# Kernel tuning notes

Measured on AMD Instinct MI355X. Metric: run time of the kernel, lower is better.

The kernel has to match this reference:

```python
import jax, jax.numpy as jnp
import numpy as np

LAMBDA_M = 1.0
NUM_GRU_LAYERS = 3

B, S, H, G = 64, 512, 768, 768


def setup_inputs() -> dict:
    key = jax.random.key(0)
    ks = jax.random.split(key, 12)
    std = 0.02
    # variable-length attention mask (all rows non-empty)
    lengths = jax.random.randint(ks[0], (B,), S // 4, S + 1)
    attention_mask = (jnp.arange(S)[None, :] < lengths[:, None]).astype(jnp.float32)
    return {
        "sentence_representation": jax.random.normal(ks[1], (B, H), jnp.float32),
        "attention_mask": attention_mask,
        "aspect_embedding": jax.random.normal(ks[2], (B, H), jnp.float32),
        "sentence_embeddings": jax.random.normal(ks[3], (B, S, H), jnp.float32),
        "ws": std * jax.random.normal(ks[4], (H, H), jnp.float32),
        "wa": std * jax.random.normal(ks[5], (H, H), jnp.float32),
        "w": std * jax.random.normal(ks[6], (H,), jnp.float32),
        "whs": std * jax.random.normal(ks[7], (H, G), jnp.float32),
        "wd1": std * jax.random.normal(ks[8], (H, H), jnp.float32),
        "wd": std * jax.random.normal(ks[9], (G, H), jnp.float32),
        "w_ih": std * jax.random.normal(ks[10], (3 * G, H), jnp.float32),  # GRU input weights (r,z,n)
        "w_hh": std * jax.random.normal(ks[11], (3 * G, G), jnp.float32),  # GRU hidden weights (r,z,n)
    }


def _gru_cell(x, h, w_ih, w_hh):
    # standard GRU cell, bias=False (torch gate order: r, z, n)
    gi = x @ w_ih.T  # (B, 3G)
    gh = h @ w_hh.T  # (B, 3G)
    i_r, i_z, i_n = jnp.split(gi, 3, axis=-1)
    h_r, h_z, h_n = jnp.split(gh, 3, axis=-1)
    r = jax.nn.sigmoid(i_r + h_r)
    z = jax.nn.sigmoid(i_z + h_z)
    n = jnp.tanh(i_n + r * h_n)
    return (1.0 - z) * n + z * h


def reference(sentence_representation, attention_mask, aspect_embedding,
              sentence_embeddings, ws, wa, w, whs, wd1, wd, w_ih, w_hh):
    # Hoist loop-invariant projections (same math as recomputing per layer)
    Se = jnp.einsum('bsh,hk->bsk', sentence_embeddings, ws)  # (B,S,H)
    A = aspect_embedding @ wa                                 # (B,H)
    mask = attention_mask                                     # (B,S)
    denom = mask.sum(-1, keepdims=True)                       # (B,1)
    h = sentence_representation
    for t in range(NUM_GRU_LAYERS):
        Wd = wd1 if t == 0 else wd
        M = Se + (h @ Wd)[:, None, :] + A[:, None, :]         # (B,S,H)
        scores = jnp.tanh(M) @ w                              # (B,S)
        m = jax.nn.softmax(LAMBDA_M * scores, axis=-1)        # (B,S)
        # reweighted masked-mean pooling
        at = jnp.einsum('bs,bsh->bh', m * mask, sentence_embeddings) / denom
        if t == 0:
            h = h @ whs                                       # project to GRU hidden dim
        h = _gru_cell(at, h, w_ih, w_hh)
    return h
```

## Files before the change

### kernel.cpp

```cpp
#include <hip/hip_runtime.h>
#include <hip/hip_bf16.h>
#include <stdint.h>

#define Bdim 64
#define Sdim 512
#define Hdim 768
#define G3   2304

typedef float f32x4 __attribute__((ext_vector_type(4)));
typedef short s16x8 __attribute__((ext_vector_type(8)));
typedef short s16x4 __attribute__((ext_vector_type(4)));

__device__ __forceinline__ float bf2f(unsigned short u){
  union { unsigned int i; float f; } c; c.i = ((unsigned int)u) << 16; return c.f;
}
__device__ __forceinline__ float bflo(unsigned int x){
  union { unsigned int i; float f; } c; c.i = x << 16; return c.f;
}
__device__ __forceinline__ float bfhi(unsigned int x){
  union { unsigned int i; float f; } c; c.i = x & 0xffff0000u; return c.f;
}
__device__ __forceinline__ unsigned short f2bf(float f){
  union { float f; unsigned int i; } c; c.f = f;
  unsigned int x = c.i;
  return (unsigned short)((x + 0x7fffu + ((x >> 16) & 1u)) >> 16);
}
__device__ __forceinline__ float fast_tanh(float x){
  float e = __expf(2.f * x);
  return 1.f - 2.f / (e + 1.f);
}
__device__ __forceinline__ float fast_sigmoid(float x){
  return 1.f / (1.f + __expf(-x));
}
__device__ __forceinline__ void gload16(const void* g, void* l){
  __builtin_amdgcn_global_load_lds((const __attribute__((address_space(1))) void*)g,
                                   (__attribute__((address_space(3))) void*)l, 16, 0, 0);
}

__global__ __launch_bounds__(256) void k_prep(const float* __restrict__ SE, unsigned short* __restrict__ SEb,
                                              const float* __restrict__ ws_, unsigned short* __restrict__ wsbT,
                                              const float* __restrict__ wd1, unsigned short* __restrict__ wd1T,
                                              const float* __restrict__ wd,  unsigned short* __restrict__ wdT,
                                              const float* __restrict__ wa,  unsigned short* __restrict__ waT,
                                              const float* __restrict__ whs, unsigned short* __restrict__ whsT,
                                              const float* __restrict__ w_ih, unsigned short* __restrict__ w_ihb,
                                              const float* __restrict__ w_hh, unsigned short* __restrict__ w_hhb,
                                              const float* __restrict__ sr,  unsigned short* __restrict__ srb,
                                              const float* __restrict__ asp, unsigned short* __restrict__ aspb){
  __shared__ float tile[64][65];
  int bid = blockIdx.x;
  if (bid < 720) {
    int which = bid / 144, r = bid % 144;
    const float* src; unsigned short* dst;
    switch (which) {
      case 0: src = ws_; dst = wsbT; break;
      case 1: src = wd1; dst = wd1T; break;
      case 2: src = wd;  dst = wdT;  break;
      case 3: src = wa;  dst = waT;  break;
      default: src = whs; dst = whsT; break;
    }
    int bx = (r % 12) * 64, by = (r / 12) * 64;
    int tx = threadIdx.x % 64, ty = threadIdx.x / 64;
    #pragma unroll
    for (int j = ty; j < 64; j += 4) tile[j][tx] = src[(size_t)(by + j) * Hdim + bx + tx];
    __syncthreads();
    #pragma unroll
    for (int j = ty; j < 64; j += 4) dst[(size_t)(bx + j) * Hdim + by + tx] = f2bf(tile[tx][j]);
    return;
  }
  bid -= 720;
  const float* s; unsigned short* d; int j;
  if      (bid < 12288) { s = SE;   d = SEb;   j = bid * 256 + threadIdx.x; }
  else if (bid < 13152) { s = w_ih; d = w_ihb; j = (bid - 12288) * 256 + threadIdx.x; }
  else if (bid < 14016) { s = w_hh; d = w_hhb; j = (bid - 13152) * 256 + threadIdx.x; }
  else if (bid < 14040) { s = sr;   d = srb;   j = (bid - 14016) * 256 + threadIdx.x; }
  else                  { s = asp;  d = aspb;  j = (bid - 14040) * 256 + threadIdx.x; }
  const float4* sp = (const float4*)s;
  float4 a = sp[2*j], b = sp[2*j+1];
  uint4 o;
  o.x = (unsigned)f2bf(a.x) | ((unsigned)f2bf(a.y) << 16);
  o.y = (unsigned)f2bf(a.z) | ((unsigned)f2bf(a.w) << 16);
  o.z = (unsigned)f2bf(b.x) | ((unsigned)f2bf(b.y) << 16);
  o.w = (unsigned)f2bf(b.z) | ((unsigned)f2bf(b.w) << 16);
  ((uint4*)d)[j] = o;
}

__global__ __launch_bounds__(256) void k_conv_bf16(const float* __restrict__ src,
                                                   unsigned short* __restrict__ dst, int n8){
  int i = blockIdx.x * 256 + threadIdx.x;
  if (i >= n8) return;
  const float4* s = (const float4*)src;
  float4 a = s[2*i], b = s[2*i+1];
  uint4 o;
  o.x = (unsigned)f2bf(a.x) | ((unsigned)f2bf(a.y) << 16);
  o.y = (unsigned)f2bf(a.z) | ((unsigned)f2bf(a.w) << 16);
  o.z = (unsigned)f2bf(b.x) | ((unsigned)f2bf(b.y) << 16);
  o.w = (unsigned)f2bf(b.z) | ((unsigned)f2bf(b.w) << 16);
  ((uint4*)dst)[i] = o;
}

__global__ __launch_bounds__(256) void k_conv4(const float* __restrict__ s0, unsigned short* __restrict__ d0, int c0,
                                               const float* __restrict__ s1, unsigned short* __restrict__ d1, int c1,
                                               const float* __restrict__ s2, unsigned short* __restrict__ d2, int c2,
                                               const float* __restrict__ s3, unsigned short* __restrict__ d3, int c3){
  int i = blockIdx.x * 256 + threadIdx.x;
  const float* s; unsigned short* d; int j;
  if (i < c0) { s = s0; d = d0; j = i; }
  else if (i < c0 + c1) { s = s1; d = d1; j = i - c0; }
  else if (i < c0 + c1 + c2) { s = s2; d = d2; j = i - c0 - c1; }
  else if (i < c0 + c1 + c2 + c3) { s = s3; d = d3; j = i - c0 - c1 - c2; }
  else return;
  const float4* sp = (const float4*)s;
  float4 a = sp[2*j], b = sp[2*j+1];
  uint4 o;
  o.x = (unsigned)f2bf(a.x) | ((unsigned)f2bf(a.y) << 16);
  o.y = (unsigned)f2bf(a.z) | ((unsigned)f2bf(a.w) << 16);
  o.z = (unsigned)f2bf(b.x) | ((unsigned)f2bf(b.y) << 16);
  o.w = (unsigned)f2bf(b.z) | ((unsigned)f2bf(b.w) << 16);
  ((uint4*)d)[j] = o;
}

__global__ __launch_bounds__(256) void k_transpose_ws(const float* __restrict__ src,
                                                      unsigned short* __restrict__ dst){
  __shared__ float tile[32][33];
  int bx = blockIdx.x * 32, by = blockIdx.y * 32;
  int tx = threadIdx.x % 32, ty = threadIdx.x / 32;
  for (int j = ty; j < 32; j += 8) tile[j][tx] = src[(size_t)(by + j) * Hdim + bx + tx];
  __syncthreads();
  for (int j = ty; j < 32; j += 8) dst[(size_t)(bx + j) * Hdim + by + tx] = f2bf(tile[tx][j]);
}

__global__ __launch_bounds__(256) void k_transpose4(const float* __restrict__ s0, unsigned short* __restrict__ d0,
                                                    const float* __restrict__ s1, unsigned short* __restrict__ d1,
                                                    const float* __restrict__ s2, unsigned short* __restrict__ d2,
                                                    const float* __restrict__ s3, unsigned short* __restrict__ d3){
  const float* src; unsigned short* dst;
  switch (blockIdx.z) {
    case 0: src = s0; dst = d0; break;
    case 1: src = s1; dst = d1; break;
    case 2: src = s2; dst = d2; break;
    default: src = s3; dst = d3; break;
  }
  __shared__ float tile[32][33];
  int bx = blockIdx.x * 32, by = blockIdx.y * 32;
  int tx = threadIdx.x % 32, ty = threadIdx.x / 32;
  for (int j = ty; j < 32; j += 8) tile[j][tx] = src[(size_t)(by + j) * Hdim + bx + tx];
  __syncthreads();
  for (int j = ty; j < 32; j += 8) dst[(size_t)(bx + j) * Hdim + by + tx] = f2bf(tile[tx][j]);
}

__global__ __launch_bounds__(256) void k_gemm_se(const unsigned short* __restrict__ A,
                                                 const unsigned short* __restrict__ Bt,
                                                 unsigned short* __restrict__ C){
  __shared__ unsigned short As[128 * 64];
  __shared__ unsigned short Bs[128 * 64];
  const int t = threadIdx.x;
  const int lane = t & 63;
  const int w = t >> 6, wr = w >> 1, wc = w & 1;
  int bid = blockIdx.x;
  int swz = (bid & 7) * 192 + (bid >> 3);
  const int m0 = (swz / 6) * 128, n0 = (swz % 6) * 128;

  f32x4 acc[4][4];
  #pragma unroll
  for (int m = 0; m < 4; m++)
    #pragma unroll
    for (int n = 0; n < 4; n++) acc[m][n] = (f32x4){0.f, 0.f, 0.f, 0.f};

  for (int k0 = 0; k0 < Hdim; k0 += 64) {
    #pragma unroll
    for (int i = 0; i < 4; i++) {
      int L = t * 16 + i * 4096;
      int row = L >> 7;
      int offp = L & 127;
      int goff = offp ^ ((row & 7) << 4);
      int wub = __builtin_amdgcn_readfirstlane((t & 192) * 16 + i * 4096);
      gload16((const char*)A  + ((size_t)(m0 + row) * Hdim + k0) * 2 + goff, (char*)As + wub);
      gload16((const char*)Bt + ((size_t)(n0 + row) * Hdim + k0) * 2 + goff, (char*)Bs + wub);
    }
    __syncthreads();
    #pragma unroll
    for (int kk = 0; kk < 2; kk++) {
      s16x8 af[4], bfr[4];
      #pragma unroll
      for (int m = 0; m < 4; m++) {
        int row = wr * 64 + m * 16 + (lane & 15);
        int sw = (row & 7) << 4;
        int kb = kk * 64 + (lane >> 4) * 8;
        s16x4 lo = *(const s16x4*)((const char*)As + row * 128 + (kb ^ sw));
        s16x4 hi = *(const s16x4*)((const char*)As + row * 128 + ((kb + 32) ^ sw));
        af[m] = __builtin_shufflevector(lo, hi, 0, 1, 2, 3, 4, 5, 6, 7);
      }
      #pragma unroll
      for (int n = 0; n < 4; n++) {
        int row = wc * 64 + n * 16 + (lane & 15);
        int sw = (row & 7) << 4;
        int kb = kk * 64 + (lane >> 4) * 8;
        s16x4 lo = *(const s16x4*)((const char*)Bs + row * 128 + (kb ^ sw));
        s16x4 hi = *(const s16x4*)((const char*)Bs + row * 128 + ((kb + 32) ^ sw));
        bfr[n] = __builtin_shufflevector(lo, hi, 0, 1, 2, 3, 4, 5, 6, 7);
      }
      #pragma unroll
      for (int m = 0; m < 4; m++)
        #pragma unroll
        for (int n = 0; n < 4; n++)
          acc[m][n] = __builtin_amdgcn_mfma_f32_16x16x32_bf16(af[m], bfr[n], acc[m][n], 0, 0, 0);
    }
    __syncthreads();
  }
  #pragma unroll
  for (int m = 0; m < 4; m++) {
    int rowb = m0 + wr * 64 + m * 16 + (lane >> 4) * 4;
    #pragma unroll
    for (int n = 0; n < 4; n++) {
      int col = n0 + wc * 64 + n * 16 + (lane & 15);
      #pragma unroll
      for (int r = 0; r < 4; r++)
        C[(size_t)(rowb + r) * Hdim + col] = f2bf(acc[m][n][r]);
    }
  }
}

__device__ __forceinline__ void smallM_body(const unsigned short* __restrict__ A,
                                            const unsigned short* __restrict__ Bt,
                                            float* __restrict__ C, unsigned short* __restrict__ Cb,
                                            char* ldsbuf, int n0){
  unsigned short* As = (unsigned short*)ldsbuf;
  unsigned short* Bs = (unsigned short*)(ldsbuf + 8192);
  const int t = threadIdx.x, lane = t & 63, w = t >> 6;
  f32x4 acc[4][2];
  #pragma unroll
  for (int m = 0; m < 4; m++)
    #pragma unroll
    for (int n = 0; n < 2; n++) acc[m][n] = (f32x4){0.f, 0.f, 0.f, 0.f};

  for (int k0 = 0; k0 < Hdim; k0 += 64) {
    #pragma unroll
    for (int i = 0; i < 2; i++) {
      int L = t * 16 + i * 4096, row = L >> 7, off = L & 127;
      *(uint4*)((char*)As + row * 128 + (off ^ ((row & 7) << 4))) =
        *(const uint4*)((const char*)A + ((size_t)row * Hdim + k0) * 2 + off);
    }
    #pragma unroll
    for (int i = 0; i < 4; i++) {
      int L = t * 16 + i * 4096, row = L >> 7, off = L & 127;
      *(uint4*)((char*)Bs + row * 128 + (off ^ ((row & 7) << 4))) =
        *(const uint4*)((const char*)Bt + ((size_t)(n0 + row) * Hdim + k0) * 2 + off);
    }
    __syncthreads();
    #pragma unroll
    for (int kk = 0; kk < 2; kk++) {
      s16x8 af[4], bfr[2];
      int kb = kk * 64 + (lane >> 4) * 8;
      #pragma unroll
      for (int m = 0; m < 4; m++) {
        int row = m * 16 + (lane & 15);
        int sw = (row & 7) << 4;
        s16x4 lo = *(const s16x4*)((const char*)As + row * 128 + (kb ^ sw));
        s16x4 hi = *(const s16x4*)((const char*)As + row * 128 + ((kb + 32) ^ sw));
        af[m] = __builtin_shufflevector(lo, hi, 0, 1, 2, 3, 4, 5, 6, 7);
      }
      #pragma unroll
      for (int n = 0; n < 2; n++) {
        int row = w * 32 + n * 16 + (lane & 15);
        int sw = (row & 7) << 4;
        s16x4 lo = *(const s16x4*)((const char*)Bs + row * 128 + (kb ^ sw));
        s16x4 hi = *(const s16x4*)((const char*)Bs + row * 128 + ((kb + 32) ^ sw));
        bfr[n] = __builtin_shufflevector(lo, hi, 0, 1, 2, 3, 4, 5, 6, 7);
      }
      #pragma unroll
      for (int m = 0; m < 4; m++)
        #pragma unroll
        for (int n = 0; n < 2; n++)
          acc[m][n] = __builtin_amdgcn_mfma_f32_16x16x32_bf16(af[m], bfr[n], acc[m][n], 0, 0, 0);
    }
    __syncthreads();
  }
  #pragma unroll
  for (int m = 0; m < 4; m++) {
    int rowb = m * 16 + (lane >> 4) * 4;
    #pragma unroll
    for (int n = 0; n < 2; n++) {
      int col = n0 + w * 32 + n * 16 + (lane & 15);
      #pragma unroll
      for (int r = 0; r < 4; r++) {
        float v = acc[m][n][r];
        C[(size_t)(rowb + r) * Hdim + col] = v;
        if (Cb) Cb[(size_t)(rowb + r) * Hdim + col] = f2bf(v);
      }
    }
  }
}

__device__ __forceinline__ void vpart_body(const unsigned short* __restrict__ A1,
                                           const unsigned short* __restrict__ B1t,
                                           const unsigned short* __restrict__ A2,
                                           const unsigned short* __restrict__ B2t,
                                           float* __restrict__ Vp,
                                           char* ldsbuf, int n0, int kc){
  unsigned short* As = (unsigned short*)ldsbuf;
  unsigned short* Bs = (unsigned short*)(ldsbuf + 8192);
  const int t = threadIdx.x, lane = t & 63, w = t >> 6;
  f32x4 acc[4][2];
  #pragma unroll
  for (int m = 0; m < 4; m++)
    #pragma unroll
    for (int n = 0; n < 2; n++) acc[m][n] = (f32x4){0.f, 0.f, 0.f, 0.f};

  #pragma unroll
  for (int gi = 0; gi < 4; gi++) {
    int g = kc * 4 + gi;
    const unsigned short* A  = (g < 12) ? A1 : A2;
    const unsigned short* Bt = (g < 12) ? B1t : B2t;
    int k0 = (g % 12) * 64;
    #pragma unroll
    for (int i = 0; i < 2; i++) {
      int L = t * 16 + i * 4096, row = L >> 7, off = L & 127;
      *(uint4*)((char*)As + row * 128 + (off ^ ((row & 7) << 4))) =
        *(const uint4*)((const char*)A + ((size_t)row * Hdim + k0) * 2 + off);
    }
    #pragma unroll
    for (int i = 0; i < 4; i++) {
      int L = t * 16 + i * 4096, row = L >> 7, off = L & 127;
      *(uint4*)((char*)Bs + row * 128 + (off ^ ((row & 7) << 4))) =
        *(const uint4*)((const char*)Bt + ((size_t)(n0 + row) * Hdim + k0) * 2 + off);
    }
    __syncthreads();
    #pragma unroll
    for (int kk = 0; kk < 2; kk++) {
      s16x8 af[4], bfr[2];
      int kb = kk * 64 + (lane >> 4) * 8;
      #pragma unroll
      for (int m = 0; m < 4; m++) {
        int row = m * 16 + (lane & 15);
        int sw = (row & 7) << 4;
        s16x4 lo = *(const s16x4*)((const char*)As + row * 128 + (kb ^ sw));
        s16x4 hi = *(const s16x4*)((const char*)As + row * 128 + ((kb + 32) ^ sw));
        af[m] = __builtin_shufflevector(lo, hi, 0, 1, 2, 3, 4, 5, 6, 7);
      }
      #pragma unroll
      for (int n = 0; n < 2; n++) {
        int row = w * 32 + n * 16 + (lane & 15);
        int sw = (row & 7) << 4;
        s16x4 lo = *(const s16x4*)((const char*)Bs + row * 128 + (kb ^ sw));
        s16x4 hi = *(const s16x4*)((const char*)Bs + row * 128 + ((kb + 32) ^ sw));
        bfr[n] = __builtin_shufflevector(lo, hi, 0, 1, 2, 3, 4, 5, 6, 7);
      }
      #pragma unroll
      for (int m = 0; m < 4; m++)
        #pragma unroll
        for (int n = 0; n < 2; n++)
          acc[m][n] = __builtin_amdgcn_mfma_f32_16x16x32_bf16(af[m], bfr[n], acc[m][n], 0, 0, 0);
    }
    __syncthreads();
  }
  float* outp = Vp + (size_t)kc * (Bdim * Hdim);
  #pragma unroll
  for (int m = 0; m < 4; m++) {
    int rowb = m * 16 + (lane >> 4) * 4;
    #pragma unroll
    for (int n = 0; n < 2; n++) {
      int col = n0 + w * 32 + n * 16 + (lane & 15);
      #pragma unroll
      for (int r = 0; r < 4; r++)
        outp[(size_t)(rowb + r) * Hdim + col] = acc[m][n][r];
    }
  }
}

__global__ __launch_bounds__(256) void k_vpart(const unsigned short* __restrict__ A1,
                                               const unsigned short* __restrict__ B1t,
                                               const unsigned short* __restrict__ A2,
                                               const unsigned short* __restrict__ B2t,
                                               float* __restrict__ Vp){
  __shared__ char lds[24576];
  vpart_body(A1, B1t, A2, B2t, Vp, lds, blockIdx.x * 128, blockIdx.y);
}

__global__ __launch_bounds__(256) void k_init2(const unsigned short* __restrict__ srb,
                                               const unsigned short* __restrict__ whsT,
                                               float* __restrict__ hA, unsigned short* __restrict__ hbA,
                                               const unsigned short* __restrict__ wd1T,
                                               const unsigned short* __restrict__ aspb,
                                               const unsigned short* __restrict__ waT,
                                               float* __restrict__ Vp){
  __shared__ char lds[24576];
  if (blockIdx.y == 6) smallM_body(srb, whsT, hA, hbA, lds, blockIdx.x * 128);
  else                 vpart_body(srb, wd1T, aspb, waT, Vp, lds, blockIdx.x * 128, blockIdx.y);
}

__global__ __launch_bounds__(256) void k_scores(const unsigned short* __restrict__ Seb,
                                                const float* __restrict__ Vp,
                                                const float* __restrict__ wv,
                                                float* __restrict__ scores){
  int b = blockIdx.y;
  int s_base = blockIdx.x * 16;
  int t = threadIdx.x, lane = t & 63, w = t >> 6;
  f32x4 v0 = {0,0,0,0}, v1 = {0,0,0,0}, v2 = {0,0,0,0};
  #pragma unroll
  for (int kc = 0; kc < 6; kc++) {
    const float* Vb = Vp + ((size_t)kc * Bdim + b) * Hdim;
    v0 += *(const f32x4*)(Vb + lane * 8);
    v1 += *(const f32x4*)(Vb + lane * 8 + 4);
    v2 += *(const f32x4*)(Vb + 512 + lane * 4);
  }
  f32x4 w0 = *(const f32x4*)(wv + lane * 8);
  f32x4 w1 = *(const f32x4*)(wv + lane * 8 + 4);
  f32x4 w2 = *(const f32x4*)(wv + 512 + lane * 4);
  #pragma unroll
  for (int si = 0; si < 4; si++) {
    int s = s_base + w * 4 + si;
    const unsigned short* rp = Seb + ((size_t)b * Sdim + s) * Hdim;
    ushort4 p0 = *(const ushort4*)(rp + lane * 8);
    ushort4 p1 = *(const ushort4*)(rp + lane * 8 + 4);
    ushort4 p2 = *(const ushort4*)(rp + 512 + lane * 4);
    float acc;
    acc  = fast_tanh(bf2f(p0.x) + v0[0]) * w0[0];
    acc += fast_tanh(bf2f(p0.y) + v0[1]) * w0[1];
    acc += fast_tanh(bf2f(p0.z) + v0[2]) * w0[2];
    acc += fast_tanh(bf2f(p0.w) + v0[3]) * w0[3];
    acc += fast_tanh(bf2f(p1.x) + v1[0]) * w1[0];
    acc += fast_tanh(bf2f(p1.y) + v1[1]) * w1[1];
    acc += fast_tanh(bf2f(p1.z) + v1[2]) * w1[2];
    acc += fast_tanh(bf2f(p1.w) + v1[3]) * w1[3];
    acc += fast_tanh(bf2f(p2.x) + v2[0]) * w2[0];
    acc += fast_tanh(bf2f(p2.y) + v2[1]) * w2[1];
    acc += fast_tanh(bf2f(p2.z) + v2[2]) * w2[2];
    acc += fast_tanh(bf2f(p2.w) + v2[3]) * w2[3];
    #pragma unroll
    for (int o = 32; o; o >>= 1) acc += __shfl_xor(acc, o);
    if (lane == 0) scores[(size_t)b * Sdim + s] = acc;
  }
}

__global__ __launch_bounds__(192) void k_at_sm_bf16(const unsigned short* __restrict__ SEb,
                                                    const float* __restrict__ scores,
                                                    const float* __restrict__ mask,
                                                    float* __restrict__ at_part){
  int sc = blockIdx.x, b = blockIdx.y;
  int t = threadIdx.x, lane = t & 63, w = t >> 6;
  __shared__ float sbuf[512];
  __shared__ float mbuf[512];
  __shared__ float red[3], red2[3];
  __shared__ float msh[32];
  __shared__ float half0[96 * 8];
  float lmax = -1e30f;
  #pragma unroll
  for (int j = 0; j < 3; j++) {
    int idx = t + 192 * j;
    if (idx < 512) {
      float v = scores[(size_t)b * Sdim + idx];
      float mk = mask[(size_t)b * Sdim + idx];
      sbuf[idx] = v; mbuf[idx] = mk;
      lmax = fmaxf(lmax, v);
    }
  }
  #pragma unroll
  for (int o = 32; o; o >>= 1) lmax = fmaxf(lmax, __shfl_xor(lmax, o));
  if (lane == 0) red[w] = lmax;
  __syncthreads();
  float mx = fmaxf(fmaxf(red[0], red[1]), red[2]);
  float le = 0.f, lm = 0.f;
  #pragma unroll
  for (int j = 0; j < 3; j++) {
    int idx = t + 192 * j;
    if (idx < 512) {
      float e = __expf(sbuf[idx] - mx);
      le += e; lm += mbuf[idx];
      sbuf[idx] = e * mbuf[idx];
    }
  }
  #pragma unroll
  for (int o = 32; o; o >>= 1) { le += __shfl_xor(le, o); lm += __shfl_xor(lm, o); }
  __syncthreads();
  if (lane == 0) { red[w] = le; red2[w] = lm; }
  __syncthreads();
  float inv = 1.f / ((red[0] + red[1] + red[2]) * (red2[0] + red2[1] + red2[2]));
  if (t < 32) msh[t] = sbuf[sc * 32 + t] * inv;
  __syncthreads();
  int hseg = t % 96, sh = t / 96;
  const unsigned short* base = SEb + ((size_t)b * Sdim + sc * 32 + sh * 16) * Hdim + hseg * 8;
  float acc[8] = {0, 0, 0, 0, 0, 0, 0, 0};
  #pragma unroll
  for (int s = 0; s < 16; s++) {
    float m = msh[sh * 16 + s];
    uint4 v = *(const uint4*)(base + (size_t)s * Hdim);
    acc[0] += m * bflo(v.x); acc[1] += m * bfhi(v.x);
    acc[2] += m * bflo(v.y); acc[3] += m * bfhi(v.y);
    acc[4] += m * bflo(v.z); acc[5] += m * bfhi(v.z);
    acc[6] += m * bflo(v.w); acc[7] += m * bfhi(v.w);
  }
  if (sh == 0) {
    #pragma unroll
    for (int j = 0; j < 8; j++) half0[hseg * 8 + j] = acc[j];
  }
  __syncthreads();
  if (sh == 1) {
    float* op = at_part + ((size_t)sc * Bdim + b) * Hdim + hseg * 8;
    #pragma unroll
    for (int j = 0; j < 8; j++) op[j] = acc[j] + half0[hseg * 8 + j];
  }
}

__global__ __launch_bounds__(192) void k_at_sm_f32(const float* __restrict__ SE,
                                                   const float* __restrict__ scores,
                                                   const float* __restrict__ mask,
                                                   float* __restrict__ at_part){
  int sc = blockIdx.x, b = blockIdx.y;
  int t = threadIdx.x, lane = t & 63, w = t >> 6;
  __shared__ float sbuf[512];
  __shared__ float mbuf[512];
  __shared__ float red[3], red2[3];
  __shared__ float msh[32];
  __shared__ float half0[96 * 8];
  float lmax = -1e30f;
  #pragma unroll
  for (int j = 0; j < 3; j++) {
    int idx = t + 192 * j;
    if (idx < 512) {
      float v = scores[(size_t)b * Sdim + idx];
      float mk = mask[(size_t)b * Sdim + idx];
      sbuf[idx] = v; mbuf[idx] = mk;
      lmax = fmaxf(lmax, v);
    }
  }
  #pragma unroll
  for (int o = 32; o; o >>= 1) lmax = fmaxf(lmax, __shfl_xor(lmax, o));
  if (lane == 0) red[w] = lmax;
  __syncthreads();
  float mx = fmaxf(fmaxf(red[0], red[1]), red[2]);
  float le = 0.f, lm = 0.f;
  #pragma unroll
  for (int j = 0; j < 3; j++) {
    int idx = t + 192 * j;
    if (idx < 512) {
      float e = __expf(sbuf[idx] - mx);
      le += e; lm += mbuf[idx];
      sbuf[idx] = e * mbuf[idx];
    }
  }
  #pragma unroll
  for (int o = 32; o; o >>= 1) { le += __shfl_xor(le, o); lm += __shfl_xor(lm, o); }
  __syncthreads();
  if (lane == 0) { red[w] = le; red2[w] = lm; }
  __syncthreads();
  float inv = 1.f / ((red[0] + red[1] + red[2]) * (red2[0] + red2[1] + red2[2]));
  if (t < 32) msh[t] = sbuf[sc * 32 + t] * inv;
  __syncthreads();
  int hseg = t % 96, sh = t / 96;
  const float* base = SE + ((size_t)b * Sdim + sc * 32 + sh * 16) * Hdim + hseg * 8;
  float acc[8] = {0, 0, 0, 0, 0, 0, 0, 0};
  #pragma unroll
  for (int s = 0; s < 16; s++) {
    float m = msh[sh * 16 + s];
    float4 a = *(const float4*)(base + (size_t)s * Hdim);
    float4 c = *(const float4*)(base + (size_t)s * Hdim + 4);
    acc[0] += m * a.x; acc[1] += m * a.y; acc[2] += m * a.z; acc[3] += m * a.w;
    acc[4] += m * c.x; acc[5] += m * c.y; acc[6] += m * c.z; acc[7] += m * c.w;
  }
  if (sh == 0) {
    #pragma unroll
    for (int j = 0; j < 8; j++) half0[hseg * 8 + j] = acc[j];
  }
  __syncthreads();
  if (sh == 1) {
    float* op = at_part + ((size_t)sc * Bdim + b) * Hdim + hseg * 8;
    #pragma unroll
    for (int j = 0; j < 8; j++) op[j] = acc[j] + half0[hseg * 8 + j];
  }
}

__global__ __launch_bounds__(256) void k_at_reduce(const float* __restrict__ at_part,
                                                   unsigned short* __restrict__ atb){
  int i = blockIdx.x * 256 + threadIdx.x;
  float s = 0.f;
  #pragma unroll
  for (int p = 0; p < 16; p++) s += at_part[(size_t)p * (Bdim * Hdim) + i];
  atb[i] = f2bf(s);
}

__global__ __launch_bounds__(256) void k_gates2(const unsigned short* __restrict__ atb,
                                                const unsigned short* __restrict__ hb,
                                                const unsigned short* __restrict__ w_ihb,
                                                const unsigned short* __restrict__ w_hhb,
                                                float* __restrict__ gi2,
                                                float* __restrict__ gh2){
  __shared__ unsigned short As[64 * 64];
  __shared__ unsigned short Bs[128 * 64];
  const int t = threadIdx.x, lane = t & 63, w = t >> 6;
  const int n0 = blockIdx.x * 128;
  const int z = blockIdx.y, kc = blockIdx.z;
  const unsigned short* A  = z ? hb : atb;
  const unsigned short* Bt = z ? w_hhb : w_ihb;
  float* outp = (z ? gh2 : gi2) + (size_t)kc * (Bdim * G3);
  f32x4 acc[4][2];
  #pragma unroll
  for (int m = 0; m < 4; m++)
    #pragma unroll
    for (int n = 0; n < 2; n++) acc[m][n] = (f32x4){0.f, 0.f, 0.f, 0.f};

  for (int it = 0; it < 6; it++) {
    int k0 = kc * 384 + it * 64;
    #pragma unroll
    for (int i = 0; i < 2; i++) {
      int L = t * 16 + i * 4096, row = L >> 7, off = L & 127;
      *(uint4*)((char*)As + row * 128 + (off ^ ((row & 7) << 4))) =
        *(const uint4*)((const char*)A + ((size_t)row * Hdim + k0) * 2 + off);
    }
    #pragma unroll
    for (int i = 0; i < 4; i++) {
      int L = t * 16 + i * 4096, row = L >> 7, off = L & 127;
      *(uint4*)((char*)Bs + row * 128 + (off ^ ((row & 7) << 4))) =
        *(const uint4*)((const char*)Bt + ((size_t)(n0 + row) * Hdim + k0) * 2 + off);
    }
    __syncthreads();
    #pragma unroll
    for (int kk = 0; kk < 2; kk++) {
      s16x8 af[4], bfr[2];
      int kb = kk * 64 + (lane >> 4) * 8;
      #pragma unroll
      for (int m = 0; m < 4; m++) {
        int row = m * 16 + (lane & 15);
        int sw = (row & 7) << 4;
        s16x4 lo = *(const s16x4*)((const char*)As + row * 128 + (kb ^ sw));
        s16x4 hi = *(const s16x4*)((const char*)As + row * 128 + ((kb + 32) ^ sw));
        af[m] = __builtin_shufflevector(lo, hi, 0, 1, 2, 3, 4, 5, 6, 7);
      }
      #pragma unroll
      for (int n = 0; n < 2; n++) {
        int row = w * 32 + n * 16 + (lane & 15);
        int sw = (row & 7) << 4;
        s16x4 lo = *(const s16x4*)((const char*)Bs + row * 128 + (kb ^ sw));
        s16x4 hi = *(const s16x4*)((const char*)Bs + row * 128 + ((kb + 32) ^ sw));
        bfr[n] = __builtin_shufflevector(lo, hi, 0, 1, 2, 3, 4, 5, 6, 7);
      }
      #pragma unroll
      for (int m = 0; m < 4; m++)
        #pragma unroll
        for (int n = 0; n < 2; n++)
          acc[m][n] = __builtin_amdgcn_mfma_f32_16x16x32_bf16(af[m], bfr[n], acc[m][n], 0, 0, 0);
    }
    __syncthreads();
  }
  #pragma unroll
  for (int m = 0; m < 4; m++) {
    int rowb = m * 16 + (lane >> 4) * 4;
    #pragma unroll
    for (int n = 0; n < 2; n++) {
      int col = n0 + w * 32 + n * 16 + (lane & 15);
      #pragma unroll
      for (int r = 0; r < 4; r++)
        outp[(size_t)(rowb + r) * G3 + col] = acc[m][n][r];
    }
  }
}

__global__ __launch_bounds__(256) void k_gru_elem2(const float* __restrict__ gi2,
                                                   const float* __restrict__ gh2,
                                                   const float* __restrict__ h,
                                                   float* __restrict__ hout,
                                                   unsigned short* __restrict__ hbout){
  int i = blockIdx.x * 256 + threadIdx.x;
  int b = i / Hdim, g = i % Hdim;
  const size_t P = (size_t)Bdim * G3;
  const float* gia = gi2 + (size_t)b * G3;
  const float* gha = gh2 + (size_t)b * G3;
  float ir = gia[g] + gia[P + g];
  float iz = gia[Hdim + g] + gia[P + Hdim + g];
  float in_ = gia[2 * Hdim + g] + gia[P + 2 * Hdim + g];
  float hr = gha[g] + gha[P + g];
  float hz = gha[Hdim + g] + gha[P + Hdim + g];
  float hn = gha[2 * Hdim + g] + gha[P + 2 * Hdim + g];
  float r = fast_sigmoid(ir + hr);
  float z = fast_sigmoid(iz + hz);
  float n = fast_tanh(in_ + r * hn);
  float ho = (1.f - z) * n + z * h[i];
  hout[i] = ho;
  hbout[i] = f2bf(ho);
}

extern "C" void kernel_launch(void* const* d_in, const int* in_sizes, int n_in,
                              void* d_out, int out_size, void* d_ws, size_t ws_size,
                              hipStream_t stream) {
  const float* sr   = (const float*)d_in[0];
  const float* mask = (const float*)d_in[1];
  const float* asp  = (const float*)d_in[2];
  const float* SE   = (const float*)d_in[3];
  const float* ws_  = (const float*)d_in[4];
  const float* wa   = (const float*)d_in[5];
  const float* wv   = (const float*)d_in[6];
  const float* whs  = (const float*)d_in[7];
  const float* wd1  = (const float*)d_in[8];
  const float* wd   = (const float*)d_in[9];
  const float* w_ih = (const float*)d_in[10];
  const float* w_hh = (const float*)d_in[11];
  float* out = (float*)d_out;

  char* p = (char*)d_ws;
  size_t offA = 0;
  auto A_ = [&](size_t b) -> char* { char* r = p + offA; offA += b; return r; };
  unsigned short* Seb  = (unsigned short*)A_(50331648);
  unsigned short* wsbT = (unsigned short*)A_(1179648);
  unsigned short* SEb  = (unsigned short*)A_(50331648);

  const size_t othersBytes = 19673088;
  bool keepSEb = (offA + othersBytes) <= ws_size;
  char* q = keepSEb ? (p + offA) : (char*)SEb;
  size_t o2 = 0;
  auto B_ = [&](size_t b) -> char* { char* r = q + o2; o2 += b; return r; };
  unsigned short* w_ihb = (unsigned short*)B_(3538944);
  unsigned short* w_hhb = (unsigned short*)B_(3538944);
  unsigned short* wd1T  = (unsigned short*)B_(1179648);
  unsigned short* wdT   = (unsigned short*)B_(1179648);
  unsigned short* waT   = (unsigned short*)B_(1179648);
  unsigned short* whsT  = (unsigned short*)B_(1179648);
  unsigned short* srb   = (unsigned short*)B_(98304);
  unsigned short* aspb  = (unsigned short*)B_(98304);
  float* Vp      = (float*)B_(1179648);
  float* scores  = (float*)B_(131072);
  float* at_part = (float*)B_(3145728);
  unsigned short* atb = (unsigned short*)B_(98304);
  float* gi2     = (float*)B_(1179648);
  float* gh2     = (float*)B_(1179648);
  float* hA      = (float*)B_(196608);
  float* hB      = (float*)B_(196608);
  unsigned short* hbA = (unsigned short*)B_(98304);
  unsigned short* hbB = (unsigned short*)B_(98304);
  if (!keepSEb && (offA > ws_size)) return;

  if (keepSEb) {
    k_prep<<<dim3(14784), dim3(256), 0, stream>>>(SE, SEb, ws_, wsbT, wd1, wd1T, wd, wdT,
                                                  wa, waT, whs, whsT, w_ih, w_ihb, w_hh, w_hhb,
                                                  sr, srb, asp, aspb);
    k_gemm_se<<<dim3(1536), dim3(256), 0, stream>>>(SEb, wsbT, Seb);
  } else {
    k_conv_bf16<<<dim3(12288), dim3(256), 0, stream>>>(SE, SEb, 3145728);
    k_transpose_ws<<<dim3(24, 24), dim3(256), 0, stream>>>(ws_, wsbT);
    k_gemm_se<<<dim3(1536), dim3(256), 0, stream>>>(SEb, wsbT, Seb);
    k_transpose4<<<dim3(24, 24, 4), dim3(256), 0, stream>>>(wd1, wd1T, wd, wdT, wa, waT, whs, whsT);
    k_conv4<<<dim3(1776), dim3(256), 0, stream>>>(w_ih, w_ihb, 221184, w_hh, w_hhb, 221184,
                                                  sr, srb, 6144, asp, aspb, 6144);
  }
  k_init2<<<dim3(6, 7), dim3(256), 0, stream>>>(srb, whsT, hA, hbA, wd1T, aspb, waT, Vp);

  const float* hcur = hA;
  const unsigned short* hbcur = hbA;
  for (int tl = 0; tl < 3; ++tl) {
    if (tl > 0)
      k_vpart<<<dim3(6, 6), dim3(256), 0, stream>>>(hbcur, wdT, aspb, waT, Vp);
    k_scores<<<dim3(32, 64), dim3(256), 0, stream>>>(Seb, Vp, wv, scores);
    if (keepSEb)
      k_at_sm_bf16<<<dim3(16, 64), dim3(192), 0, stream>>>(SEb, scores, mask, at_part);
    else
      k_at_sm_f32<<<dim3(16, 64), dim3(192), 0, stream>>>(SE, scores, mask, at_part);
    k_at_reduce<<<dim3(192), dim3(256), 0, stream>>>(at_part, atb);
    k_gates2<<<dim3(18, 2, 2), dim3(256), 0, stream>>>(atb, hbcur, w_ihb, w_hhb, gi2, gh2);
    float* hout = (tl == 2) ? out : ((hcur == hA) ? hB : hA);
    unsigned short* hbout = (hbcur == hbA) ? hbB : hbA;
    k_gru_elem2<<<dim3(192), dim3(256), 0, stream>>>(gi2, gh2, hcur, hout, hbout);
    hcur = hout;
    hbcur = hbout;
  }
}
```

Baseline: 236.0 us.

## Fuse at-reduce, gate GEMMs, GRU update and vpart into one cooperative kernel

Replaces the per-layer sequence of four small kernels (at_reduce, gates GEMM, GRU elementwise, next-layer vpart) with one cooperative launch of 72 blocks that separates the stages with grid-wide syncs. The goal is to cut kernel launch gaps and tail latency in the small, latency-bound recurrent part. In exchange, it pays for grid.sync barriers and leaves fewer blocks for the elementwise stages.

```diff
diff --git a/kernel.cpp b/kernel.cpp
--- a/kernel.cpp
+++ b/kernel.cpp
@@ -1,6 +1,9 @@
 #include <hip/hip_runtime.h>
 #include <hip/hip_bf16.h>
+#include <hip/hip_cooperative_groups.h>
 #include <stdint.h>
+
+namespace cg = cooperative_groups;
 
 #define Bdim 64
 #define Sdim 512
@@ -368,13 +371,73 @@
   }
 }
 
-__global__ __launch_bounds__(256) void k_vpart(const unsigned short* __restrict__ A1,
-                                               const unsigned short* __restrict__ B1t,
-                                               const unsigned short* __restrict__ A2,
-                                               const unsigned short* __restrict__ B2t,
-                                               float* __restrict__ Vp){
-  __shared__ char lds[24576];
-  vpart_body(A1, B1t, A2, B2t, Vp, lds, blockIdx.x * 128, blockIdx.y);
+__device__ __forceinline__ void gates_body(const unsigned short* __restrict__ A,
+                                           const unsigned short* __restrict__ Bt,
+                                           float* __restrict__ outp,
+                                           char* ldsbuf, int n0, int kc){
+  unsigned short* As = (unsigned short*)ldsbuf;
+  unsigned short* Bs = (unsigned short*)(ldsbuf + 8192);
+  const int t = threadIdx.x, lane = t & 63, w = t >> 6;
+  f32x4 acc[4][2];
+  #pragma unroll
+  for (int m = 0; m < 4; m++)
+    #pragma unroll
+    for (int n = 0; n < 2; n++) acc[m][n] = (f32x4){0.f, 0.f, 0.f, 0.f};
+
+  for (int it = 0; it < 6; it++) {
+    int k0 = kc * 384 + it * 64;
+    #pragma unroll
+    for (int i = 0; i < 2; i++) {
+      int L = t * 16 + i * 4096, row = L >> 7, off = L & 127;
+      *(uint4*)((char*)As + row * 128 + (off ^ ((row & 7) << 4))) =
+        *(const uint4*)((const char*)A + ((size_t)row * Hdim + k0) * 2 + off);
+    }
+    #pragma unroll
+    for (int i = 0; i < 4; i++) {
+      int L = t * 16 + i * 4096, row = L >> 7, off = L & 127;
+      *(uint4*)((char*)Bs + row * 128 + (off ^ ((row & 7) << 4))) =
+        *(const uint4*)((const char*)Bt + ((size_t)(n0 + row) * Hdim + k0) * 2 + off);
+    }
+    __syncthreads();
+    #pragma unroll
+    for (int kk = 0; kk < 2; kk++) {
+      s16x8 af[4], bfr[2];
+      int kb = kk * 64 + (lane >> 4) * 8;
+      #pragma unroll
+      for (int m = 0; m < 4; m++) {
+        int row = m * 16 + (lane & 15);
+        int sw = (row & 7) << 4;
+        s16x4 lo = *(const s16x4*)((const char*)As + row * 128 + (kb ^ sw));
+        s16x4 hi = *(const s16x4*)((const char*)As + row * 128 + ((kb + 32) ^ sw));
+        af[m] = __builtin_shufflevector(lo, hi, 0, 1, 2, 3, 4, 5, 6, 7);
+      }
+      #pragma unroll
+      for (int n = 0; n < 2; n++) {
+        int row = w * 32 + n * 16 + (lane & 15);
+        int sw = (row & 7) << 4;
+        s16x4 lo = *(const s16x4*)((const char*)Bs + row * 128 + (kb ^ sw));
+        s16x4 hi = *(const s16x4*)((const char*)Bs + row * 128 + ((kb + 32) ^ sw));
+        bfr[n] = __builtin_shufflevector(lo, hi, 0, 1, 2, 3, 4, 5, 6, 7);
+      }
+      #pragma unroll
+      for (int m = 0; m < 4; m++)
+        #pragma unroll
+        for (int n = 0; n < 2; n++)
+          acc[m][n] = __builtin_amdgcn_mfma_f32_16x16x32_bf16(af[m], bfr[n], acc[m][n], 0, 0, 0);
+    }
+    __syncthreads();
+  }
+  #pragma unroll
+  for (int m = 0; m < 4; m++) {
+    int rowb = m * 16 + (lane >> 4) * 4;
+    #pragma unroll
+    for (int n = 0; n < 2; n++) {
+      int col = n0 + w * 32 + n * 16 + (lane & 15);
+      #pragma unroll
+      for (int r = 0; r < 4; r++)
+        outp[(size_t)(rowb + r) * G3 + col] = acc[m][n][r];
+    }
+  }
 }
 
 __global__ __launch_bounds__(256) void k_init2(const unsigned short* __restrict__ srb,
@@ -570,113 +633,53 @@
   }
 }
 
-__global__ __launch_bounds__(256) void k_at_reduce(const float* __restrict__ at_part,
-                                                   unsigned short* __restrict__ atb){
-  int i = blockIdx.x * 256 + threadIdx.x;
-  float s = 0.f;
-  #pragma unroll
-  for (int p = 0; p < 16; p++) s += at_part[(size_t)p * (Bdim * Hdim) + i];
-  atb[i] = f2bf(s);
-}
-
-__global__ __launch_bounds__(256) void k_gates2(const unsigned short* __restrict__ atb,
-                                                const unsigned short* __restrict__ hb,
-                                                const unsigned short* __restrict__ w_ihb,
-                                                const unsigned short* __restrict__ w_hhb,
-                                                float* __restrict__ gi2,
-                                                float* __restrict__ gh2){
-  __shared__ unsigned short As[64 * 64];
-  __shared__ unsigned short Bs[128 * 64];
-  const int t = threadIdx.x, lane = t & 63, w = t >> 6;
-  const int n0 = blockIdx.x * 128;
-  const int z = blockIdx.y, kc = blockIdx.z;
-  const unsigned short* A  = z ? hb : atb;
-  const unsigned short* Bt = z ? w_hhb : w_ihb;
-  float* outp = (z ? gh2 : gi2) + (size_t)kc * (Bdim * G3);
-  f32x4 acc[4][2];
-  #pragma unroll
-  for (int m = 0; m < 4; m++)
-    #pragma unroll
-    for (int n = 0; n < 2; n++) acc[m][n] = (f32x4){0.f, 0.f, 0.f, 0.f};
-
-  for (int it = 0; it < 6; it++) {
-    int k0 = kc * 384 + it * 64;
-    #pragma unroll
-    for (int i = 0; i < 2; i++) {
-      int L = t * 16 + i * 4096, row = L >> 7, off = L & 127;
-      *(uint4*)((char*)As + row * 128 + (off ^ ((row & 7) << 4))) =
-        *(const uint4*)((const char*)A + ((size_t)row * Hdim + k0) * 2 + off);
-    }
-    #pragma unroll
-    for (int i = 0; i < 4; i++) {
-      int L = t * 16 + i * 4096, row = L >> 7, off = L & 127;
-      *(uint4*)((char*)Bs + row * 128 + (off ^ ((row & 7) << 4))) =
-        *(const uint4*)((const char*)Bt + ((size_t)(n0 + row) * Hdim + k0) * 2 + off);
-    }
-    __syncthreads();
-    #pragma unroll
-    for (int kk = 0; kk < 2; kk++) {
-      s16x8 af[4], bfr[2];
-      int kb = kk * 64 + (lane >> 4) * 8;
-      #pragma unroll
-      for (int m = 0; m < 4; m++) {
-        int row = m * 16 + (lane & 15);
-        int sw = (row & 7) << 4;
-        s16x4 lo = *(const s16x4*)((const char*)As + row * 128 + (kb ^ sw));
-        s16x4 hi = *(const s16x4*)((const char*)As + row * 128 + ((kb + 32) ^ sw));
-        af[m] = __builtin_shufflevector(lo, hi, 0, 1, 2, 3, 4, 5, 6, 7);
-      }
-      #pragma unroll
-      for (int n = 0; n < 2; n++) {
-        int row = w * 32 + n * 16 + (lane & 15);
-        int sw = (row & 7) << 4;
-        s16x4 lo = *(const s16x4*)((const char*)Bs + row * 128 + (kb ^ sw));
-        s16x4 hi = *(const s16x4*)((const char*)Bs + row * 128 + ((kb + 32) ^ sw));
-        bfr[n] = __builtin_shufflevector(lo, hi, 0, 1, 2, 3, 4, 5, 6, 7);
-      }
-      #pragma unroll
-      for (int m = 0; m < 4; m++)
-        #pragma unroll
-        for (int n = 0; n < 2; n++)
-          acc[m][n] = __builtin_amdgcn_mfma_f32_16x16x32_bf16(af[m], bfr[n], acc[m][n], 0, 0, 0);
-    }
-    __syncthreads();
-  }
-  #pragma unroll
-  for (int m = 0; m < 4; m++) {
-    int rowb = m * 16 + (lane >> 4) * 4;
-    #pragma unroll
-    for (int n = 0; n < 2; n++) {
-      int col = n0 + w * 32 + n * 16 + (lane & 15);
-      #pragma unroll
-      for (int r = 0; r < 4; r++)
-        outp[(size_t)(rowb + r) * G3 + col] = acc[m][n][r];
-    }
-  }
-}
-
-__global__ __launch_bounds__(256) void k_gru_elem2(const float* __restrict__ gi2,
-                                                   const float* __restrict__ gh2,
-                                                   const float* __restrict__ h,
-                                                   float* __restrict__ hout,
-                                                   unsigned short* __restrict__ hbout){
-  int i = blockIdx.x * 256 + threadIdx.x;
-  int b = i / Hdim, g = i % Hdim;
+__global__ __launch_bounds__(256) void k_tail(const float* at_part, unsigned short* atb,
+                                              const unsigned short* hb,
+                                              const unsigned short* w_ihb, const unsigned short* w_hhb,
+                                              float* gi2, float* gh2,
+                                              const float* h, float* hout, unsigned short* hbout,
+                                              const unsigned short* wdT, const unsigned short* aspb,
+                                              const unsigned short* waT, float* Vp, int do_vpart){
+  cg::grid_group grid = cg::this_grid();
+  __shared__ char lds[24576];
+  const int bid = blockIdx.x, t = threadIdx.x;
+  for (int i = bid * 256 + t; i < Bdim * Hdim; i += 72 * 256) {
+    float s = 0.f;
+    #pragma unroll
+    for (int p = 0; p < 16; p++) s += at_part[(size_t)p * (Bdim * Hdim) + i];
+    atb[i] = f2bf(s);
+  }
+  grid.sync();
+  if (bid < 36) {
+    gates_body(atb, w_ihb, gi2 + (size_t)(bid / 18) * (Bdim * G3), lds, (bid % 18) * 128, bid / 18);
+  } else {
+    int b2 = bid - 36;
+    gates_body(hb, w_hhb, gh2 + (size_t)(b2 / 18) * (Bdim * G3), lds, (b2 % 18) * 128, b2 / 18);
+  }
+  grid.sync();
   const size_t P = (size_t)Bdim * G3;
-  const float* gia = gi2 + (size_t)b * G3;
-  const float* gha = gh2 + (size_t)b * G3;
-  float ir = gia[g] + gia[P + g];
-  float iz = gia[Hdim + g] + gia[P + Hdim + g];
-  float in_ = gia[2 * Hdim + g] + gia[P + 2 * Hdim + g];
-  float hr = gha[g] + gha[P + g];
-  float hz = gha[Hdim + g] + gha[P + Hdim + g];
-  float hn = gha[2 * Hdim + g] + gha[P + 2 * Hdim + g];
-  float r = fast_sigmoid(ir + hr);
-  float z = fast_sigmoid(iz + hz);
-  float n = fast_tanh(in_ + r * hn);
-  float ho = (1.f - z) * n + z * h[i];
-  hout[i] = ho;
-  hbout[i] = f2bf(ho);
+  for (int i = bid * 256 + t; i < Bdim * Hdim; i += 72 * 256) {
+    int b = i / Hdim, g = i % Hdim;
+    const float* gia = gi2 + (size_t)b * G3;
+    const float* gha = gh2 + (size_t)b * G3;
+    float ir = gia[g] + gia[P + g];
+    float iz = gia[Hdim + g] + gia[P + Hdim + g];
+    float in_ = gia[2 * Hdim + g] + gia[P + 2 * Hdim + g];
+    float hr = gha[g] + gha[P + g];
+    float hz = gha[Hdim + g] + gha[P + Hdim + g];
+    float hn = gha[2 * Hdim + g] + gha[P + 2 * Hdim + g];
+    float r = fast_sigmoid(ir + hr);
+    float z = fast_sigmoid(iz + hz);
+    float n = fast_tanh(in_ + r * hn);
+    float ho = (1.f - z) * n + z * h[i];
+    hout[i] = ho;
+    hbout[i] = f2bf(ho);
+  }
+  if (do_vpart) {
+    grid.sync();
+    if (bid < 36)
+      vpart_body(hbout, wdT, aspb, waT, Vp, lds, (bid % 6) * 128, bid / 6);
+  }
 }
 
 extern "C" void kernel_launch(void* const* d_in, const int* in_sizes, int n_in,
@@ -746,18 +749,25 @@
   const float* hcur = hA;
   const unsigned short* hbcur = hbA;
   for (int tl = 0; tl < 3; ++tl) {
-    if (tl > 0)
-      k_vpart<<<dim3(6, 6), dim3(256), 0, stream>>>(hbcur, wdT, aspb, waT, Vp);
     k_scores<<<dim3(32, 64), dim3(256), 0, stream>>>(Seb, Vp, wv, scores);
     if (keepSEb)
       k_at_sm_bf16<<<dim3(16, 64), dim3(192), 0, stream>>>(SEb, scores, mask, at_part);
     else
       k_at_sm_f32<<<dim3(16, 64), dim3(192), 0, stream>>>(SE, scores, mask, at_part);
-    k_at_reduce<<<dim3(192), dim3(256), 0, stream>>>(at_part, atb);
-    k_gates2<<<dim3(18, 2, 2), dim3(256), 0, stream>>>(atb, hbcur, w_ihb, w_hhb, gi2, gh2);
     float* hout = (tl == 2) ? out : ((hcur == hA) ? hB : hA);
     unsigned short* hbout = (hbcur == hbA) ? hbB : hbA;
-    k_gru_elem2<<<dim3(192), dim3(256), 0, stream>>>(gi2, gh2, hcur, hout, hbout);
+    const float* atp = at_part; unsigned short* atbp = atb;
+    const unsigned short* hbp = hbcur;
+    const unsigned short* wihp = w_ihb; const unsigned short* whhp = w_hhb;
+    float* gip = gi2; float* ghp = gh2;
+    const float* hp = hcur; float* houtp = hout; unsigned short* hboutp = hbout;
+    const unsigned short* wdTp = wdT; const unsigned short* aspbp = aspb;
+    const unsigned short* waTp = waT; float* Vpp = Vp;
+    int dovp = (tl < 2) ? 1 : 0;
+    void* kargs[] = {(void*)&atp, (void*)&atbp, (void*)&hbp, (void*)&wihp, (void*)&whhp,
+                     (void*)&gip, (void*)&ghp, (void*)&hp, (void*)&houtp, (void*)&hboutp,
+                     (void*)&wdTp, (void*)&aspbp, (void*)&waTp, (void*)&Vpp, (void*)&dovp};
+    hipLaunchCooperativeKernel((void*)k_tail, dim3(72), dim3(256), kargs, 0, stream);
     hcur = hout;
     hbcur = hbout;
   }
```

Measured after the change: 360.5 us. 52.8% more time.

## Fuse fp32-to-bf16 conversion of sentence embeddings into the Se GEMM A-tile load

Applied to the files above, without the earlier changes.

The separate pass that converted the full sentence_embeddings tensor to bf16 is removed. The Se projection GEMM now reads fp32 A directly, converts it in registers, and writes the tile into swizzled LDS. Blocks with n0==0 also write the bf16 copy out for later use. This saves one full write+read round trip of the bf16 tensor and a kernel launch. In exchange, the GEMM's A loads become synchronous register loads instead of async global-to-LDS loads, and each fp32 A tile is re-read by all six column blocks at twice the bytes.

```diff
diff --git a/kernel.cpp b/kernel.cpp
--- a/kernel.cpp
+++ b/kernel.cpp
@@ -37,8 +37,7 @@
                                    (__attribute__((address_space(3))) void*)l, 16, 0, 0);
 }
 
-__global__ __launch_bounds__(256) void k_prep(const float* __restrict__ SE, unsigned short* __restrict__ SEb,
-                                              const float* __restrict__ ws_, unsigned short* __restrict__ wsbT,
+__global__ __launch_bounds__(256) void k_prep(const float* __restrict__ ws_, unsigned short* __restrict__ wsbT,
                                               const float* __restrict__ wd1, unsigned short* __restrict__ wd1T,
                                               const float* __restrict__ wd,  unsigned short* __restrict__ wdT,
                                               const float* __restrict__ wa,  unsigned short* __restrict__ waT,
@@ -70,11 +69,10 @@
   }
   bid -= 720;
   const float* s; unsigned short* d; int j;
-  if      (bid < 12288) { s = SE;   d = SEb;   j = bid * 256 + threadIdx.x; }
-  else if (bid < 13152) { s = w_ih; d = w_ihb; j = (bid - 12288) * 256 + threadIdx.x; }
-  else if (bid < 14016) { s = w_hh; d = w_hhb; j = (bid - 13152) * 256 + threadIdx.x; }
-  else if (bid < 14040) { s = sr;   d = srb;   j = (bid - 14016) * 256 + threadIdx.x; }
-  else                  { s = asp;  d = aspb;  j = (bid - 14040) * 256 + threadIdx.x; }
+  if      (bid < 864)  { s = w_ih; d = w_ihb; j = bid * 256 + threadIdx.x; }
+  else if (bid < 1728) { s = w_hh; d = w_hhb; j = (bid - 864) * 256 + threadIdx.x; }
+  else if (bid < 1752) { s = sr;   d = srb;   j = (bid - 1728) * 256 + threadIdx.x; }
+  else                 { s = asp;  d = aspb;  j = (bid - 1752) * 256 + threadIdx.x; }
   const float4* sp = (const float4*)s;
   float4 a = sp[2*j], b = sp[2*j+1];
   uint4 o;
@@ -85,73 +83,10 @@
   ((uint4*)d)[j] = o;
 }
 
-__global__ __launch_bounds__(256) void k_conv_bf16(const float* __restrict__ src,
-                                                   unsigned short* __restrict__ dst, int n8){
-  int i = blockIdx.x * 256 + threadIdx.x;
-  if (i >= n8) return;
-  const float4* s = (const float4*)src;
-  float4 a = s[2*i], b = s[2*i+1];
-  uint4 o;
-  o.x = (unsigned)f2bf(a.x) | ((unsigned)f2bf(a.y) << 16);
-  o.y = (unsigned)f2bf(a.z) | ((unsigned)f2bf(a.w) << 16);
-  o.z = (unsigned)f2bf(b.x) | ((unsigned)f2bf(b.y) << 16);
-  o.w = (unsigned)f2bf(b.z) | ((unsigned)f2bf(b.w) << 16);
-  ((uint4*)dst)[i] = o;
-}
-
-__global__ __launch_bounds__(256) void k_conv4(const float* __restrict__ s0, unsigned short* __restrict__ d0, int c0,
-                                               const float* __restrict__ s1, unsigned short* __restrict__ d1, int c1,
-                                               const float* __restrict__ s2, unsigned short* __restrict__ d2, int c2,
-                                               const float* __restrict__ s3, unsigned short* __restrict__ d3, int c3){
-  int i = blockIdx.x * 256 + threadIdx.x;
-  const float* s; unsigned short* d; int j;
-  if (i < c0) { s = s0; d = d0; j = i; }
-  else if (i < c0 + c1) { s = s1; d = d1; j = i - c0; }
-  else if (i < c0 + c1 + c2) { s = s2; d = d2; j = i - c0 - c1; }
-  else if (i < c0 + c1 + c2 + c3) { s = s3; d = d3; j = i - c0 - c1 - c2; }
-  else return;
-  const float4* sp = (const float4*)s;
-  float4 a = sp[2*j], b = sp[2*j+1];
-  uint4 o;
-  o.x = (unsigned)f2bf(a.x) | ((unsigned)f2bf(a.y) << 16);
-  o.y = (unsigned)f2bf(a.z) | ((unsigned)f2bf(a.w) << 16);
-  o.z = (unsigned)f2bf(b.x) | ((unsigned)f2bf(b.y) << 16);
-  o.w = (unsigned)f2bf(b.z) | ((unsigned)f2bf(b.w) << 16);
-  ((uint4*)d)[j] = o;
-}
-
-__global__ __launch_bounds__(256) void k_transpose_ws(const float* __restrict__ src,
-                                                      unsigned short* __restrict__ dst){
-  __shared__ float tile[32][33];
-  int bx = blockIdx.x * 32, by = blockIdx.y * 32;
-  int tx = threadIdx.x % 32, ty = threadIdx.x / 32;
-  for (int j = ty; j < 32; j += 8) tile[j][tx] = src[(size_t)(by + j) * Hdim + bx + tx];
-  __syncthreads();
-  for (int j = ty; j < 32; j += 8) dst[(size_t)(bx + j) * Hdim + by + tx] = f2bf(tile[tx][j]);
-}
-
-__global__ __launch_bounds__(256) void k_transpose4(const float* __restrict__ s0, unsigned short* __restrict__ d0,
-                                                    const float* __restrict__ s1, unsigned short* __restrict__ d1,
-                                                    const float* __restrict__ s2, unsigned short* __restrict__ d2,
-                                                    const float* __restrict__ s3, unsigned short* __restrict__ d3){
-  const float* src; unsigned short* dst;
-  switch (blockIdx.z) {
-    case 0: src = s0; dst = d0; break;
-    case 1: src = s1; dst = d1; break;
-    case 2: src = s2; dst = d2; break;
-    default: src = s3; dst = d3; break;
-  }
-  __shared__ float tile[32][33];
-  int bx = blockIdx.x * 32, by = blockIdx.y * 32;
-  int tx = threadIdx.x % 32, ty = threadIdx.x / 32;
-  for (int j = ty; j < 32; j += 8) tile[j][tx] = src[(size_t)(by + j) * Hdim + bx + tx];
-  __syncthreads();
-  for (int j = ty; j < 32; j += 8) dst[(size_t)(bx + j) * Hdim + by + tx] = f2bf(tile[tx][j]);
-}
-
-__global__ __launch_bounds__(256) void k_gemm_se(const unsigned short* __restrict__ A,
+__global__ __launch_bounds__(256) void k_gemm_se(const float* __restrict__ A32,
                                                  const unsigned short* __restrict__ Bt,
-                                                 unsigned short* __restrict__ C){
+                                                 unsigned short* __restrict__ C,
+                                                 unsigned short* __restrict__ SEbOut){
   __shared__ unsigned short As[128 * 64];
   __shared__ unsigned short Bs[128 * 64];
   const int t = threadIdx.x;
@@ -160,6 +95,7 @@
   int bid = blockIdx.x;
   int swz = (bid & 7) * 192 + (bid >> 3);
   const int m0 = (swz / 6) * 128, n0 = (swz % 6) * 128;
+  const bool wr_seb = (SEbOut != nullptr) && (n0 == 0);
 
   f32x4 acc[4][4];
   #pragma unroll
@@ -172,10 +108,20 @@
     for (int i = 0; i < 4; i++) {
       int L = t * 16 + i * 4096;
       int row = L >> 7;
-      int offp = L & 127;
-      int goff = offp ^ ((row & 7) << 4);
+      int off = L & 127;
+      int e0 = off >> 1;
+      const float* srcp = A32 + ((size_t)(m0 + row) * Hdim + k0 + e0);
+      float4 a = *(const float4*)(srcp);
+      float4 b = *(const float4*)(srcp + 4);
+      uint4 o;
+      o.x = (unsigned)f2bf(a.x) | ((unsigned)f2bf(a.y) << 16);
+      o.y = (unsigned)f2bf(a.z) | ((unsigned)f2bf(a.w) << 16);
+      o.z = (unsigned)f2bf(b.x) | ((unsigned)f2bf(b.y) << 16);
+      o.w = (unsigned)f2bf(b.z) | ((unsigned)f2bf(b.w) << 16);
+      *(uint4*)((char*)As + row * 128 + (off ^ ((row & 7) << 4))) = o;
+      if (wr_seb) *(uint4*)(SEbOut + (size_t)(m0 + row) * Hdim + k0 + e0) = o;
+      int goff = off ^ ((row & 7) << 4);
       int wub = __builtin_amdgcn_readfirstlane((t & 192) * 16 + i * 4096);
-      gload16((const char*)A  + ((size_t)(m0 + row) * Hdim + k0) * 2 + goff, (char*)As + wub);
       gload16((const char*)Bt + ((size_t)(n0 + row) * Hdim + k0) * 2 + goff, (char*)Bs + wub);
     }
     __syncthreads();
@@ -728,19 +674,10 @@
   unsigned short* hbB = (unsigned short*)B_(98304);
   if (!keepSEb && (offA > ws_size)) return;
 
-  if (keepSEb) {
-    k_prep<<<dim3(14784), dim3(256), 0, stream>>>(SE, SEb, ws_, wsbT, wd1, wd1T, wd, wdT,
-                                                  wa, waT, whs, whsT, w_ih, w_ihb, w_hh, w_hhb,
-                                                  sr, srb, asp, aspb);
-    k_gemm_se<<<dim3(1536), dim3(256), 0, stream>>>(SEb, wsbT, Seb);
-  } else {
-    k_conv_bf16<<<dim3(12288), dim3(256), 0, stream>>>(SE, SEb, 3145728);
-    k_transpose_ws<<<dim3(24, 24), dim3(256), 0, stream>>>(ws_, wsbT);
-    k_gemm_se<<<dim3(1536), dim3(256), 0, stream>>>(SEb, wsbT, Seb);
-    k_transpose4<<<dim3(24, 24, 4), dim3(256), 0, stream>>>(wd1, wd1T, wd, wdT, wa, waT, whs, whsT);
-    k_conv4<<<dim3(1776), dim3(256), 0, stream>>>(w_ih, w_ihb, 221184, w_hh, w_hhb, 221184,
-                                                  sr, srb, 6144, asp, aspb, 6144);
-  }
+  k_prep<<<dim3(2496), dim3(256), 0, stream>>>(ws_, wsbT, wd1, wd1T, wd, wdT,
+                                               wa, waT, whs, whsT, w_ih, w_ihb, w_hh, w_hhb,
+                                               sr, srb, asp, aspb);
+  k_gemm_se<<<dim3(1536), dim3(256), 0, stream>>>(SE, wsbT, Seb, keepSEb ? SEb : nullptr);
   k_init2<<<dim3(6, 7), dim3(256), 0, stream>>>(srb, whsT, hA, hbA, wd1T, aspb, waT, Vp);
 
   const float* hcur = hA;
```

Result: slower. 269.3 us (+14.1%).
